# Kernel tuning notes

Measured on AMD Instinct MI355X. Metric: run time of the kernel, lower is better.

## Reference

```python
import jax, jax.numpy as jnp
import numpy as np

N = 8192      # source grid points
M = 8192      # output grid points
NB = 16       # n_basis
WIDTH = 32    # int(n_basis * enhancement)
EPS = 1e-4
LOG2 = 0.6931471805599453


def log_cosh(x):
    a = jnp.abs(x)
    return a + jnp.log1p(jnp.exp(-2.0 * a)) - LOG2


def setup_inputs() -> dict:
    key = jax.random.key(0)
    ks = jax.random.split(key, 9)
    rho = jax.random.uniform(ks[0], (N,), minval=0.05, maxval=2.0)
    gamma = jax.random.uniform(ks[1], (N,), minval=0.01, maxval=1.0)
    coords = jax.random.normal(ks[2], (N, 3)) * 5.0
    weights = jax.random.uniform(ks[3], (N,), minval=0.0, maxval=0.1)
    out_coords = jax.random.normal(ks[4], (M, 3)) * 5.0
    # field_embed params: Linear(1 -> WIDTH), Linear(WIDTH -> NB)
    w1 = jax.random.normal(ks[5], (1, WIDTH)) * 1.0
    b1 = jax.random.normal(ks[6], (WIDTH,)) * 0.1
    w2 = jax.random.normal(ks[7], (WIDTH, NB)) / np.sqrt(WIDTH)
    b2 = jax.random.normal(ks[8], (NB,)) * 0.1
    return {"rho": rho, "gamma": gamma, "coords": coords, "weights": weights,
            "out_coords": out_coords, "w1": w1, "b1": b1, "w2": w2, "b2": b2}


def _field_embed(x, w1, b1, w2, b2):
    # x: (..., 1) -> (..., NB)
    return jnp.tanh(x @ w1 + b1) @ w2 + b2


def reference(rho, gamma, coords, weights, out_coords, w1, b1, w2, b2):
    # rescaled (reduced) density gradient s^2 = gamma / (4 (3 pi^2)^{2/3} rho^{8/3})
    s2 = gamma / (4.0 * (3.0 * jnp.pi ** 2) ** (2.0 / 3.0) * rho ** (8.0 / 3.0))
    x = jnp.log(s2 + EPS)[:, None]                     # (N, 1)
    exponent = log_cosh(_field_embed(x, w1, b1, w2, b2))  # (N, NB)
    heg_scale = log_cosh(_field_embed(jnp.zeros((1, 1), rho.dtype), w1, b1, w2, b2)) ** 1.5  # (1, NB)
    beta = jnp.pi * (rho[:, None] / 2.0) ** (2.0 / 3.0) * exponent  # (N, NB)
    wrho = weights * rho                                # (N,)

    # all-pairs squared distances (M, N), computed once
    d2 = (jnp.sum(out_coords ** 2, axis=1)[:, None]
          + jnp.sum(coords ** 2, axis=1)[None, :]
          - 2.0 * out_coords @ coords.T)
    d2 = jnp.maximum(d2, 0.0)

    # KeOps Genred: y[i, b] = sum_j exp(-beta[j, b] * d2[i, j]) * wrho[j]
    # scan over the (small, fixed) basis axis so only one (M, N) kernel slice lives at a time
    def body(carry, beta_b):                            # beta_b: (N,)
        yb = jnp.exp(-d2 * beta_b[None, :]) @ wrho      # (M,)
        return carry, yb

    _, ys = jax.lax.scan(body, 0, beta.T)               # (NB, M)
    return ys.T * heg_scale                             # (M, NB)
```

## Files before the change

### kernel.cpp

```cpp
#include <hip/hip_runtime.h>
#include <hip/hip_bf16.h>


#define N_PTS 8192
#define M_PTS 8192
#define NBASIS 16
#define WIDTH 32

typedef float v2f __attribute__((ext_vector_type(2)));

__device__ __forceinline__ float exp2_hw(float x) { return __builtin_amdgcn_exp2f(x); }
__device__ __forceinline__ float log2_hw(float x) { return __builtin_amdgcn_logf(x); }

__device__ __forceinline__ float fast_tanh(float z) {
    float a = fabsf(z);
    float t = __expf(-2.0f * a);
    float r = (1.0f - t) / (1.0f + t);
    return copysignf(r, z);
}

__device__ __forceinline__ float log_cosh_f(float x) {
    float a = fabsf(x);
    return a + __logf(1.0f + __expf(-2.0f * a)) - 0.6931471805599453f;
}

__global__ __launch_bounds__(64)
void cg_prep(const float* __restrict__ rho,
             const float* __restrict__ gamma,
             const float* __restrict__ coords,
             const float* __restrict__ weights,
             const float* __restrict__ w1,
             const float* __restrict__ b1,
             const float* __restrict__ w2,
             const float* __restrict__ b2,
             float4* __restrict__ cw,
             float4* __restrict__ bnq,
             float* __restrict__ hegf)
{
    const float PI_F = 3.14159265358979323846f;
    const float LOG2E = 1.4426950408889634f;

    __shared__ float s_w1[WIDTH], s_b1[WIDTH], s_w2[WIDTH * NBASIS], s_b2[NBASIS];
    int t = threadIdx.x;
    if (t < WIDTH) { s_w1[t] = w1[t]; s_b1[t] = b1[t]; }
    if (t < NBASIS) s_b2[t] = b2[t];
    #pragma unroll
    for (int k = 0; k < 8; ++k) s_w2[t + 64 * k] = w2[t + 64 * k];
    __syncthreads();

    int j = blockIdx.x * 64 + t;
    {
        float r = rho[j];
        float g = gamma[j];
        const float c83 = 38.28312007948569f;
        float r83 = exp2_hw(2.6666666667f * log2_hw(r));
        float s2 = g / (c83 * r83);
        float x = __logf(s2 + 1e-4f);

        float emb[NBASIS];
        #pragma unroll
        for (int b = 0; b < NBASIS; ++b) emb[b] = s_b2[b];
        #pragma unroll 4
        for (int w = 0; w < WIDTH; ++w) {
            float h = fast_tanh(fmaf(x, s_w1[w], s_b1[w]));
            #pragma unroll
            for (int b = 0; b < NBASIS; ++b)
                emb[b] = fmaf(h, s_w2[w * NBASIS + b], emb[b]);
        }
        float pref = PI_F * exp2_hw(0.6666666667f * log2_hw(0.5f * r));
        float scale = -LOG2E * pref;
        #pragma unroll
        for (int q = 0; q < 4; ++q) {
            bnq[q * N_PTS + j] = make_float4(scale * log_cosh_f(emb[4 * q + 0]),
                                             scale * log_cosh_f(emb[4 * q + 1]),
                                             scale * log_cosh_f(emb[4 * q + 2]),
                                             scale * log_cosh_f(emb[4 * q + 3]));
        }

        cw[j] = make_float4(coords[j * 3 + 0],
                            coords[j * 3 + 1],
                            coords[j * 3 + 2],
                            weights[j] * r);
    }

    if (blockIdx.x == 0 && t == 0) {
        float emb0[NBASIS];
        #pragma unroll
        for (int b = 0; b < NBASIS; ++b) emb0[b] = s_b2[b];
        for (int w = 0; w < WIDTH; ++w) {
            float h = fast_tanh(s_b1[w]);
            #pragma unroll
            for (int b = 0; b < NBASIS; ++b)
                emb0[b] = fmaf(h, s_w2[w * NBASIS + b], emb0[b]);
        }
        #pragma unroll
        for (int b = 0; b < NBASIS; ++b) {
            float lc = fmaxf(log_cosh_f(emb0[b]), 0.0f);
            hegf[b] = lc * sqrtf(lc);
        }
    }
}

__global__ __launch_bounds__(256, 4)
void cg_pairs(const float* __restrict__ oc,
              const float4* __restrict__ cw,
              const float4* __restrict__ bnq,
              const float* __restrict__ hegf,
              float* __restrict__ out)
{
    int wave = (blockIdx.x << 2) | (threadIdx.x >> 6);
    int lane = threadIdx.x & 63;
    int i0 = wave << 1;
    int i1 = i0 | 1;

    v2f oxv = { oc[i0 * 3 + 0], oc[i1 * 3 + 0] };
    v2f oyv = { oc[i0 * 3 + 1], oc[i1 * 3 + 1] };
    v2f ozv = { oc[i0 * 3 + 2], oc[i1 * 3 + 2] };

    v2f acc[NBASIS];
    #pragma unroll
    for (int b = 0; b < NBASIS; ++b) acc[b] = (v2f)0.0f;

    #pragma unroll 2
    for (int k = 0; k < N_PTS / 64; ++k) {
        int j = (k << 6) | lane;
        float4 c = cw[j];
        v2f dx = oxv - c.x;
        v2f dy = oyv - c.y;
        v2f dz = ozv - c.z;
        v2f d2 = dx * dx + dy * dy + dz * dz;
        #pragma unroll
        for (int q = 0; q < 4; ++q) {
            float4 b4 = bnq[q * N_PTS + j];
            v2f p0 = b4.x * d2;
            v2f p1 = b4.y * d2;
            v2f p2 = b4.z * d2;
            v2f p3 = b4.w * d2;
            v2f e0 = { exp2_hw(p0.x), exp2_hw(p0.y) };
            v2f e1 = { exp2_hw(p1.x), exp2_hw(p1.y) };
            v2f e2 = { exp2_hw(p2.x), exp2_hw(p2.y) };
            v2f e3 = { exp2_hw(p3.x), exp2_hw(p3.y) };
            acc[q * 4 + 0] += e0 * c.w;
            acc[q * 4 + 1] += e1 * c.w;
            acc[q * 4 + 2] += e2 * c.w;
            acc[q * 4 + 3] += e3 * c.w;
        }
    }

    #pragma unroll
    for (int m = 1; m < 64; m <<= 1) {
        #pragma unroll
        for (int b = 0; b < NBASIS; ++b) {
            v2f other = { __shfl_xor(acc[b].x, m, 64),
                          __shfl_xor(acc[b].y, m, 64) };
            acc[b] += other;
        }
    }

    if (lane == 0) {
        #pragma unroll
        for (int b = 0; b < NBASIS; ++b) {
            float h = hegf[b];
            out[i0 * NBASIS + b] = acc[b].x * h;
            out[i1 * NBASIS + b] = acc[b].y * h;
        }
    }
}

extern "C" void kernel_launch(void* const* d_in, const int* in_sizes, int n_in,
                              void* d_out, int out_size, void* d_ws, size_t ws_size,
                              hipStream_t stream) {
    const float* rho        = (const float*)d_in[0];
    const float* gamma      = (const float*)d_in[1];
    const float* coords     = (const float*)d_in[2];
    const float* weights    = (const float*)d_in[3];
    const float* out_coords = (const float*)d_in[4];
    const float* w1         = (const float*)d_in[5];
    const float* b1         = (const float*)d_in[6];
    const float* w2         = (const float*)d_in[7];
    const float* b2         = (const float*)d_in[8];

    char* ws = (char*)d_ws;
    float4* cw   = (float4*)(ws);
    float4* bnq  = (float4*)(ws + (128 << 10));
    float*  hegf = (float*) (ws + (640 << 10));

    cg_prep<<<N_PTS / 64, 64, 0, stream>>>(rho, gamma, coords, weights,
                                           w1, b1, w2, b2,
                                           cw, bnq, hegf);

    cg_pairs<<<M_PTS / 8, 256, 0, stream>>>(out_coords, cw, bnq, hegf,
                                            (float*)d_out);
}
```

Measured before the change: 190.6 us.

## Split source-point reduction into two halves with a combine kernel

The pairs kernel now splits the N source points into two halves, doubling the grid to 2048 blocks so each wave reduces over 4096 points. Partial sums for the second half go to a workspace buffer, and a new combine kernel adds the two halves and applies the heg scale. Launch bounds are raised to 8 waves per EU to allow higher occupancy, which may force register spilling given 32 accumulator floats. The split adds a third launch and an extra pass over the output in exchange for more parallelism.

New measurement: 216.8 us. 1.14x slower.

```diff
diff --git a/kernel.cpp b/kernel.cpp
--- a/kernel.cpp
+++ b/kernel.cpp
@@ -101,17 +101,20 @@
     }
 }
 
-__global__ __launch_bounds__(256, 4)
+__global__ __launch_bounds__(256, 8)
 void cg_pairs(const float* __restrict__ oc,
               const float4* __restrict__ cw,
               const float4* __restrict__ bnq,
-              const float* __restrict__ hegf,
-              float* __restrict__ out)
+              float* __restrict__ out,
+              float* __restrict__ ypart)
 {
-    int wave = (blockIdx.x << 2) | (threadIdx.x >> 6);
+    int wid  = (blockIdx.x << 2) | (threadIdx.x >> 6);
     int lane = threadIdx.x & 63;
-    int i0 = wave << 1;
+    int half = wid >> 12;
+    int pair = wid & 4095;
+    int i0 = pair << 1;
     int i1 = i0 | 1;
+    int jbase = half << 12;
 
     v2f oxv = { oc[i0 * 3 + 0], oc[i1 * 3 + 0] };
     v2f oyv = { oc[i0 * 3 + 1], oc[i1 * 3 + 1] };
@@ -122,8 +125,8 @@
     for (int b = 0; b < NBASIS; ++b) acc[b] = (v2f)0.0f;
 
     #pragma unroll 2
-    for (int k = 0; k < N_PTS / 64; ++k) {
-        int j = (k << 6) | lane;
+    for (int k = 0; k < 64; ++k) {
+        int j = jbase + (k << 6) + lane;
         float4 c = cw[j];
         v2f dx = oxv - c.x;
         v2f dy = oyv - c.y;
@@ -158,13 +161,22 @@
     }
 
     if (lane == 0) {
+        float* dst = half ? ypart : out;
         #pragma unroll
         for (int b = 0; b < NBASIS; ++b) {
-            float h = hegf[b];
-            out[i0 * NBASIS + b] = acc[b].x * h;
-            out[i1 * NBASIS + b] = acc[b].y * h;
-        }
-    }
+            dst[i0 * NBASIS + b] = acc[b].x;
+            dst[i1 * NBASIS + b] = acc[b].y;
+        }
+    }
+}
+
+__global__ __launch_bounds__(256)
+void cg_combine(float* __restrict__ out,
+                const float* __restrict__ ypart,
+                const float* __restrict__ hegf)
+{
+    int idx = blockIdx.x * blockDim.x + threadIdx.x;
+    out[idx] = (out[idx] + ypart[idx]) * hegf[idx & (NBASIS - 1)];
 }
 
 extern "C" void kernel_launch(void* const* d_in, const int* in_sizes, int n_in,
@@ -181,14 +193,18 @@
     const float* b2         = (const float*)d_in[8];
 
     char* ws = (char*)d_ws;
-    float4* cw   = (float4*)(ws);
-    float4* bnq  = (float4*)(ws + (128 << 10));
-    float*  hegf = (float*) (ws + (640 << 10));
+    float4* cw    = (float4*)(ws);
+    float4* bnq   = (float4*)(ws + (128 << 10));
+    float*  ypart = (float*) (ws + (640 << 10));
+    float*  hegf  = (float*) (ws + (1152 << 10));
 
     cg_prep<<<N_PTS / 64, 64, 0, stream>>>(rho, gamma, coords, weights,
                                            w1, b1, w2, b2,
                                            cw, bnq, hegf);
 
-    cg_pairs<<<M_PTS / 8, 256, 0, stream>>>(out_coords, cw, bnq, hegf,
-                                            (float*)d_out);
-}
+    cg_pairs<<<M_PTS / 4, 256, 0, stream>>>(out_coords, cw, bnq,
+                                            (float*)d_out, ypart);
+
+    cg_combine<<<(M_PTS * NBASIS) / 256, 256, 0, stream>>>((float*)d_out,
+                                                           ypart, hegf);
+}
```

## Fuse prep and pair kernels into one launch with a global flag barrier

Applied to the files above, without the earlier changes.

Merges the preprocessing kernel into the pairwise kernel. The first 32 blocks compute the embeddings and packed coordinates, then signal completion through an atomic counter, and every block spins on that counter before running the pairwise sum. This removes one kernel launch and the gap between launches, at the cost of a hipMemset per call, spin-wait overhead, and a risk of deadlock if the prep blocks are not scheduled before the waiting blocks fill the device.

New measurement: 246.7 us. +29.4%, slower.

```diff
diff --git a/kernel.cpp b/kernel.cpp
--- a/kernel.cpp
+++ b/kernel.cpp
@@ -6,6 +6,7 @@
 #define M_PTS 8192
 #define NBASIS 16
 #define WIDTH 32
+#define PREP_BLOCKS 32
 
 typedef float v2f __attribute__((ext_vector_type(2)));
 
@@ -24,92 +25,101 @@
     return a + __logf(1.0f + __expf(-2.0f * a)) - 0.6931471805599453f;
 }
 
-__global__ __launch_bounds__(64)
-void cg_prep(const float* __restrict__ rho,
-             const float* __restrict__ gamma,
-             const float* __restrict__ coords,
-             const float* __restrict__ weights,
-             const float* __restrict__ w1,
-             const float* __restrict__ b1,
-             const float* __restrict__ w2,
-             const float* __restrict__ b2,
-             float4* __restrict__ cw,
-             float4* __restrict__ bnq,
-             float* __restrict__ hegf)
+__global__ __launch_bounds__(256, 4)
+void cg_all(const float* __restrict__ rho,
+            const float* __restrict__ gamma,
+            const float* __restrict__ coords,
+            const float* __restrict__ weights,
+            const float* __restrict__ oc,
+            const float* __restrict__ w1,
+            const float* __restrict__ b1,
+            const float* __restrict__ w2,
+            const float* __restrict__ b2,
+            float4* __restrict__ cw,
+            float4* __restrict__ bnq,
+            float* __restrict__ hegf,
+            int* __restrict__ flag,
+            float* __restrict__ out)
 {
     const float PI_F = 3.14159265358979323846f;
     const float LOG2E = 1.4426950408889634f;
-
-    __shared__ float s_w1[WIDTH], s_b1[WIDTH], s_w2[WIDTH * NBASIS], s_b2[NBASIS];
     int t = threadIdx.x;
-    if (t < WIDTH) { s_w1[t] = w1[t]; s_b1[t] = b1[t]; }
-    if (t < NBASIS) s_b2[t] = b2[t];
-    #pragma unroll
-    for (int k = 0; k < 8; ++k) s_w2[t + 64 * k] = w2[t + 64 * k];
+
+    if (blockIdx.x < PREP_BLOCKS) {
+        __shared__ float s_w1[WIDTH], s_b1[WIDTH], s_w2[WIDTH * NBASIS], s_b2[NBASIS];
+        if (t < WIDTH) { s_w1[t] = w1[t]; s_b1[t] = b1[t]; }
+        if (t < NBASIS) s_b2[t] = b2[t];
+        s_w2[t] = w2[t];
+        s_w2[t + 256] = w2[t + 256];
+        __syncthreads();
+
+        int j = blockIdx.x * 256 + t;
+        {
+            float r = rho[j];
+            float g = gamma[j];
+            const float c83 = 38.28312007948569f;
+            float r83 = exp2_hw(2.6666666667f * log2_hw(r));
+            float s2 = g / (c83 * r83);
+            float x = __logf(s2 + 1e-4f);
+
+            float emb[NBASIS];
+            #pragma unroll
+            for (int b = 0; b < NBASIS; ++b) emb[b] = s_b2[b];
+            #pragma unroll 4
+            for (int w = 0; w < WIDTH; ++w) {
+                float h = fast_tanh(fmaf(x, s_w1[w], s_b1[w]));
+                #pragma unroll
+                for (int b = 0; b < NBASIS; ++b)
+                    emb[b] = fmaf(h, s_w2[w * NBASIS + b], emb[b]);
+            }
+            float pref = PI_F * exp2_hw(0.6666666667f * log2_hw(0.5f * r));
+            float scale = -LOG2E * pref;
+            #pragma unroll
+            for (int q = 0; q < 4; ++q) {
+                bnq[q * N_PTS + j] = make_float4(scale * log_cosh_f(emb[4 * q + 0]),
+                                                 scale * log_cosh_f(emb[4 * q + 1]),
+                                                 scale * log_cosh_f(emb[4 * q + 2]),
+                                                 scale * log_cosh_f(emb[4 * q + 3]));
+            }
+            cw[j] = make_float4(coords[j * 3 + 0],
+                                coords[j * 3 + 1],
+                                coords[j * 3 + 2],
+                                weights[j] * r);
+        }
+
+        if (blockIdx.x == 0 && t == 0) {
+            float emb0[NBASIS];
+            #pragma unroll
+            for (int b = 0; b < NBASIS; ++b) emb0[b] = s_b2[b];
+            for (int w = 0; w < WIDTH; ++w) {
+                float h = fast_tanh(s_b1[w]);
+                #pragma unroll
+                for (int b = 0; b < NBASIS; ++b)
+                    emb0[b] = fmaf(h, s_w2[w * NBASIS + b], emb0[b]);
+            }
+            #pragma unroll
+            for (int b = 0; b < NBASIS; ++b) {
+                float lc = fmaxf(log_cosh_f(emb0[b]), 0.0f);
+                hegf[b] = lc * sqrtf(lc);
+            }
+        }
+
+        __threadfence();
+        __syncthreads();
+        if (t == 0)
+            __hip_atomic_fetch_add(flag, 1, __ATOMIC_RELEASE,
+                                   __HIP_MEMORY_SCOPE_AGENT);
+    }
+
+    if (t == 0) {
+        while (__hip_atomic_load(flag, __ATOMIC_ACQUIRE,
+                                 __HIP_MEMORY_SCOPE_AGENT) < PREP_BLOCKS)
+            __builtin_amdgcn_s_sleep(8);
+    }
     __syncthreads();
 
-    int j = blockIdx.x * 64 + t;
-    {
-        float r = rho[j];
-        float g = gamma[j];
-        const float c83 = 38.28312007948569f;
-        float r83 = exp2_hw(2.6666666667f * log2_hw(r));
-        float s2 = g / (c83 * r83);
-        float x = __logf(s2 + 1e-4f);
-
-        float emb[NBASIS];
-        #pragma unroll
-        for (int b = 0; b < NBASIS; ++b) emb[b] = s_b2[b];
-        #pragma unroll 4
-        for (int w = 0; w < WIDTH; ++w) {
-            float h = fast_tanh(fmaf(x, s_w1[w], s_b1[w]));
-            #pragma unroll
-            for (int b = 0; b < NBASIS; ++b)
-                emb[b] = fmaf(h, s_w2[w * NBASIS + b], emb[b]);
-        }
-        float pref = PI_F * exp2_hw(0.6666666667f * log2_hw(0.5f * r));
-        float scale = -LOG2E * pref;
-        #pragma unroll
-        for (int q = 0; q < 4; ++q) {
-            bnq[q * N_PTS + j] = make_float4(scale * log_cosh_f(emb[4 * q + 0]),
-                                             scale * log_cosh_f(emb[4 * q + 1]),
-                                             scale * log_cosh_f(emb[4 * q + 2]),
-                                             scale * log_cosh_f(emb[4 * q + 3]));
-        }
-
-        cw[j] = make_float4(coords[j * 3 + 0],
-                            coords[j * 3 + 1],
-                            coords[j * 3 + 2],
-                            weights[j] * r);
-    }
-
-    if (blockIdx.x == 0 && t == 0) {
-        float emb0[NBASIS];
-        #pragma unroll
-        for (int b = 0; b < NBASIS; ++b) emb0[b] = s_b2[b];
-        for (int w = 0; w < WIDTH; ++w) {
-            float h = fast_tanh(s_b1[w]);
-            #pragma unroll
-            for (int b = 0; b < NBASIS; ++b)
-                emb0[b] = fmaf(h, s_w2[w * NBASIS + b], emb0[b]);
-        }
-        #pragma unroll
-        for (int b = 0; b < NBASIS; ++b) {
-            float lc = fmaxf(log_cosh_f(emb0[b]), 0.0f);
-            hegf[b] = lc * sqrtf(lc);
-        }
-    }
-}
-
-__global__ __launch_bounds__(256, 4)
-void cg_pairs(const float* __restrict__ oc,
-              const float4* __restrict__ cw,
-              const float4* __restrict__ bnq,
-              const float* __restrict__ hegf,
-              float* __restrict__ out)
-{
-    int wave = (blockIdx.x << 2) | (threadIdx.x >> 6);
-    int lane = threadIdx.x & 63;
+    int wave = (blockIdx.x << 2) | (t >> 6);
+    int lane = t & 63;
     int i0 = wave << 1;
     int i1 = i0 | 1;
 
@@ -184,11 +194,12 @@
     float4* cw   = (float4*)(ws);
     float4* bnq  = (float4*)(ws + (128 << 10));
     float*  hegf = (float*) (ws + (640 << 10));
-
-    cg_prep<<<N_PTS / 64, 64, 0, stream>>>(rho, gamma, coords, weights,
-                                           w1, b1, w2, b2,
-                                           cw, bnq, hegf);
-
-    cg_pairs<<<M_PTS / 8, 256, 0, stream>>>(out_coords, cw, bnq, hegf,
-                                            (float*)d_out);
-}
+    int*    flag = (int*)   (ws + (640 << 10) + 256);
+
+    (void)hipMemsetAsync(flag, 0, sizeof(int), stream);
+
+    cg_all<<<M_PTS / 8, 256, 0, stream>>>(rho, gamma, coords, weights,
+                                          out_coords, w1, b1, w2, b2,
+                                          cw, bnq, hegf, flag,
+                                          (float*)d_out);
+}
```
